# Optimization experiments

Measured on AMD Instinct MI355X. Metric: run time of the kernel, lower is better.

The kernel has to match this reference:

```python
import jax, jax.numpy as jnp
from jax import lax
import numpy as np

NUM_BLOCKS = 50
HIDDEN = 16
KERNEL = 9  # padding = 4 -> 'SAME' for stride 1
B, H, W = 16, 128, 128


def setup_inputs() -> dict:
    key = jax.random.key(0)
    k0, k1, k2, k3, k4 = jax.random.split(key, 5)
    x = jax.random.normal(k0, (B, 1, H, W), jnp.float32)
    # Stacked per-block params; block i uses w1[i, :, :1+i] (rest is padding, never read)
    w1 = jax.random.normal(k1, (NUM_BLOCKS, HIDDEN, 1 + NUM_BLOCKS, KERNEL, KERNEL), jnp.float32) * 0.05
    b1 = jax.random.normal(k2, (NUM_BLOCKS, HIDDEN), jnp.float32) * 0.05
    w2 = jax.random.normal(k3, (NUM_BLOCKS, HIDDEN), jnp.float32) * 0.05  # 1x1 conv to 1 channel
    b2 = jax.random.normal(k4, (NUM_BLOCKS,), jnp.float32) * 0.05
    return {"x": x, "w1": w1, "b1": b1, "w2": w2, "b2": b2}


def reference(x, w1, b1, w2, b2):
    # DenseNet-style growing concat: block i consumes concat of x and all previous outputs.
    feats = x  # [B, 1+i, H, W] at block i
    outs = []
    for i in range(NUM_BLOCKS):
        wi = w1[i, :, : 1 + i]  # [HIDDEN, 1+i, K, K]
        h = lax.conv_general_dilated(
            feats, wi, window_strides=(1, 1), padding="SAME",
            dimension_numbers=("NCHW", "OIHW", "NCHW"))
        h = jax.nn.relu(h + b1[i][None, :, None, None])  # [B, HIDDEN, H, W]
        # 1x1 conv to a single channel + sigmoid
        y = jax.nn.sigmoid(jnp.einsum("bchw,c->bhw", h, w2[i])[:, None] + b2[i])  # [B,1,H,W]
        outs.append(y)
        feats = jnp.concatenate([feats, y], axis=1)
    # Original returns a list of 50 [B,1,H,W] tensors; concatenate along channel dim.
    return jnp.concatenate(outs, axis=1)  # [B, NUM_BLOCKS, H, W]
```

## Files before the change

### kernel.cpp

```cpp
#include <hip/hip_runtime.h>
#include <hip/hip_bf16.h>

#define NBLK 50
#define HID  16
#define BATCH 16
#define HH 128
#define WW 128
#define PH 136
#define PW 136
#define NCH 2
#define PXS 32
#define ROWE (PW*PXS)
#define TAPE 512

typedef __attribute__((ext_vector_type(8))) short short8;
typedef __attribute__((ext_vector_type(4))) float floatx4;

static __device__ __forceinline__ unsigned short f2bf(float f) {
    unsigned int u = __float_as_uint(f);
    unsigned int r = (u + 0x7fffu + ((u >> 16) & 1u)) >> 16;
    return (unsigned short)r;
}

static __device__ __forceinline__ int uswz(int v) { return v ^ ((v >> 3) & 7); }
static __device__ __forceinline__ int swz(int px, int kg) { return uswz(px * 4 + kg); }

#define GLD16(gp, lp) __builtin_amdgcn_global_load_lds( \
    (__attribute__((address_space(1))) void*)(void*)(gp), \
    (__attribute__((address_space(3))) void*)(lp), 16, 0, 0)

static __device__ __forceinline__ void stage_row_u(
    const unsigned short* g, unsigned short* l, int tid,
    int NU, int sh, int um1) {
    #pragma unroll
    for (int t = 0; t < 3; ++t) {
        int j = t * 256 + tid;
        if (j < NU) {
            int v  = uswz(j);
            int pg = ((v >> sh) << 2) + (v & um1);
            GLD16((const char*)g + (size_t)uswz(pg) * 16,
                  (char*)l + (size_t)(t * 256 + (tid & ~63)) * 16);
        }
    }
}

__global__ void prep_w(const float* __restrict__ w1, unsigned short* __restrict__ wbuf) {
    int idx = blockIdx.x * 256 + threadIdx.x;
    const int total = NBLK * NCH * 81 * TAPE;
    if (idx >= total) return;
    int e    = idx & 7;
    int lane = (idx >> 3) & 63;
    int slot = (idx >> 9) % 81;
    int bc   = idx / (81 * TAPE);
    int ch   = bc & 1, blk = bc >> 1;
    int hc   = lane & 15, kg = lane >> 4;
    int Kc = blk + 1 - 32 * ch;
    if (Kc > 32) Kc = 32;
    float v = 0.f;
    if (Kc >= 1) {
        int kgs = (Kc + 7) >> 3;
        int sh  = (kgs >= 3) ? 2 : (kgs >> 1);
        int P   = 4 >> sh;
        int ky  = slot / 9, q = slot % 9;
        int kx  = q * P + (kg >> sh);
        int cl  = (kg & ((1 << sh) - 1)) * 8 + e;
        int c   = ch * 32 + cl;
        if (kx <= 8 && c <= blk)
            v = w1[(((size_t)blk * HID + hc) * (1 + NBLK) + c) * 81 + ky * 9 + kx];
    }
    wbuf[idx] = f2bf(v);
}

__global__ void zero_halo(unsigned short* __restrict__ feats) {
    int t = blockIdx.x * 256 + threadIdx.x;
    const int PPX = 2112;
    const int TOT = BATCH * NCH * PPX * 4;
    if (t >= TOT) return;
    int w    = t & 3;
    int rest = t >> 2;
    int p    = rest % PPX;
    int ch   = (rest / PPX) % NCH;
    int b    = rest / (PPX * NCH);
    int row, px;
    if (p < 1088) {
        int r4 = p / 136; px = p % 136;
        row = (r4 < 4) ? r4 : r4 + 128;
    } else {
        int q = p - 1088;
        row = 4 + (q >> 3);
        int c = q & 7;
        px = (c < 4) ? c : c + 128;
    }
    float4* dst = (float4*)((char*)feats +
        ((((size_t)b * PH + row) * NCH + ch) * ROWE) * 2 + (size_t)swz(px, w) * 16);
    *dst = make_float4(0.f, 0.f, 0.f, 0.f);
}

__global__ void init_x(const float* __restrict__ x, unsigned short* __restrict__ feats) {
    int idx = blockIdx.x * 256 + threadIdx.x;
    if (idx >= BATCH * HH * WW) return;
    int xw = idx & (WW - 1);
    int yy = (idx >> 7) & (HH - 1);
    int b  = idx >> 14;
    int pp = xw + 4;
    feats[((((size_t)b * PH + (yy + 4)) * NCH)) * ROWE + (size_t)swz(pp, 0) * 8]
        = f2bf(x[idx]);
}

template<int SH>
static __device__ __forceinline__ void chunk_pass(
    const unsigned short* __restrict__ base,
    const unsigned short* __restrict__ wsrc,
    unsigned short (*sB)[ROWE],
    floatx4 (&acc)[4][2],
    int tid, int n, int kg, int x0)
{
    constexpr int P   = 4 >> SH;
    constexpr int PT  = (8 + P) / P;
    constexpr int um1 = (1 << SH) - 1;
    constexpr int NU  = 136 << SH;
    const int bvx = ((x0 + n + (kg >> SH)) << SH) + (kg & um1);
    const size_t rstride = (size_t)NCH * ROWE;

    if constexpr (SH < 2) {
        if (tid < 16)
            *(short8*)(&sB[tid >> 3][(size_t)(NU + (tid & 7)) * 8]) =
                (short8){0, 0, 0, 0, 0, 0, 0, 0};
    }

    short8 Areg[4][PT];
    stage_row_u(base, &sB[0][0], tid, NU, SH, um1);
    #pragma unroll
    for (int q = 0; q < PT; ++q)
        Areg[0][q] = *(const short8*)(wsrc + (size_t)q * TAPE);
    __syncthreads();

    #pragma unroll
    for (int step = 0; step < 12; ++step) {
        if (step < 11)
            stage_row_u(base + (size_t)(step + 1) * rstride,
                        &sB[(step + 1) & 1][0], tid, NU, SH, um1);

        const unsigned short* bb = &sB[step & 1][0];
        #pragma unroll
        for (int q = 0; q < PT; ++q) {
            short8 B0 = *(const short8*)(bb + (size_t)uswz(bvx + 4 * q) * 8);
            short8 B1 = *(const short8*)(bb + (size_t)uswz(bvx + (16 << SH) + 4 * q) * 8);
            #pragma unroll
            for (int o = 0; o < 4; ++o) {
                if (o <= step && step - o <= 8) {
                    acc[o][0] = __builtin_amdgcn_mfma_f32_16x16x32_bf16(
                        Areg[(step - o) & 3][q], B0, acc[o][0], 0, 0, 0);
                    acc[o][1] = __builtin_amdgcn_mfma_f32_16x16x32_bf16(
                        Areg[(step - o) & 3][q], B1, acc[o][1], 0, 0, 0);
                }
            }
        }

        if (step < 8) {
            #pragma unroll
            for (int q = 0; q < PT; ++q)
                Areg[(step + 1) & 3][q] =
                    *(const short8*)(wsrc + (size_t)((step + 1) * 9 + q) * TAPE);
        }
        __syncthreads();
    }
}

__global__ __launch_bounds__(256, 2) void block_kern(
    unsigned short* feats, const unsigned short* __restrict__ wbuf,
    const float* __restrict__ b1, const float* __restrict__ w2,
    const float* __restrict__ b2, float* __restrict__ out,
    int blk, int nchunk)
{
    __shared__ __align__(16) unsigned short sB[2][ROWE];

    const int xcd = blockIdx.x & 7;
    const int i   = blockIdx.x >> 3;
    const int b   = 2 * xcd + (i >> 5);
    const int s   = i & 31;

    const int tid  = threadIdx.x;
    const int lane = tid & 63;
    const int wv   = tid >> 6;
    const int n    = lane & 15;
    const int kg   = lane >> 4;
    const int x0   = wv * 32;

    floatx4 acc[4][2];
    #pragma unroll
    for (int o = 0; o < 4; ++o)
        #pragma unroll
        for (int t = 0; t < 2; ++t)
            acc[o][t] = (floatx4){0.f, 0.f, 0.f, 0.f};

    const unsigned short* fb = feats + (size_t)b * PH * NCH * ROWE;

    for (int c = 0; c < nchunk; ++c) {
        const unsigned short* wsrc = wbuf + (size_t)(blk * NCH + c) * 81 * TAPE + lane * 8;
        const unsigned short* base = fb + (size_t)((4 * s) * NCH + c) * ROWE;
        int Kc = blk + 1 - 32 * c;
        if (Kc > 32) Kc = 32;
        const int kgs = (Kc + 7) >> 3;
        if (kgs >= 3)      chunk_pass<2>(base, wsrc, sB, acc, tid, n, kg, x0);
        else if (kgs == 2) chunk_pass<1>(base, wsrc, sB, acc, tid, n, kg, x0);
        else               chunk_pass<0>(base, wsrc, sB, acc, tid, n, kg, x0);
    }

    float b1v[4], w2v[4];
    #pragma unroll
    for (int r = 0; r < 4; ++r) {
        b1v[r] = b1[blk * HID + kg * 4 + r];
        w2v[r] = w2[blk * HID + kg * 4 + r];
    }
    const float bb2 = b2[blk];
    const int cw = blk + 1, cchunk = cw >> 5, cidx = cw & 31;

    #pragma unroll
    for (int o = 0; o < 4; ++o) {
        const int yrow = 4 * s + o;
        #pragma unroll
        for (int t = 0; t < 2; ++t) {
            float p = 0.f;
            #pragma unroll
            for (int r = 0; r < 4; ++r)
                p += fmaxf(acc[o][t][r] + b1v[r], 0.f) * w2v[r];
            p += __shfl_xor(p, 16, 64);
            p += __shfl_xor(p, 32, 64);
            if (kg == 0) {
                float yv = 1.f / (1.f + __expf(-(p + bb2)));
                int px = x0 + 16 * t + n;
                out[(((size_t)b * NBLK + blk) * HH + yrow) * WW + px] = yv;
                int pp = px + 4;
                feats[(((size_t)b * PH + (yrow + 4)) * NCH + cchunk) * ROWE
                      + (size_t)swz(pp, cidx >> 3) * 8 + (cidx & 7)] = f2bf(yv);
            }
        }
    }
}

extern "C" void kernel_launch(void* const* d_in, const int* in_sizes, int n_in,
                              void* d_out, int out_size, void* d_ws, size_t ws_size,
                              hipStream_t stream) {
    const float* x  = (const float*)d_in[0];
    const float* w1 = (const float*)d_in[1];
    const float* b1 = (const float*)d_in[2];
    const float* w2 = (const float*)d_in[3];
    const float* b2 = (const float*)d_in[4];
    float* out = (float*)d_out;

    unsigned short* feats = (unsigned short*)d_ws;
    size_t feats_bytes = (size_t)BATCH * PH * NCH * ROWE * sizeof(unsigned short);
    unsigned short* wbuf = (unsigned short*)((char*)d_ws + feats_bytes);

    const int htotal = BATCH * NCH * 2112 * 4;
    zero_halo<<<(htotal + 255) / 256, 256, 0, stream>>>(feats);
    init_x<<<(BATCH * HH * WW + 255) / 256, 256, 0, stream>>>(x, feats);
    const int wtotal = NBLK * NCH * 81 * TAPE;
    prep_w<<<(wtotal + 255) / 256, 256, 0, stream>>>(w1, wbuf);

    for (int blk = 0; blk < NBLK; ++blk) {
        int nchunk = (blk + 32) / 32;
        block_kern<<<BATCH * 32, 256, 0, stream>>>(feats, wbuf, b1, w2, b2, out, blk, nchunk);
    }
}
```

Before: 1.170 ms.

## Process two input rows per barrier with a four-slot LDS ring

```diff
diff --git a/kernel.cpp b/kernel.cpp
--- a/kernel.cpp
+++ b/kernel.cpp
@@ -123,48 +123,59 @@
     const size_t rstride = (size_t)NCH * ROWE;
 
     if constexpr (SH < 2) {
-        if (tid < 16)
+        if (tid < 32)
             *(short8*)(&sB[tid >> 3][(size_t)(NU + (tid & 7)) * 8]) =
                 (short8){0, 0, 0, 0, 0, 0, 0, 0};
     }
 
     short8 Areg[4][PT];
-    stage_row_u(base, &sB[0][0], tid, NU, SH, um1);
+    stage_row_u(base,           &sB[0][0], tid, NU, SH, um1);
+    stage_row_u(base + rstride, &sB[1][0], tid, NU, SH, um1);
     #pragma unroll
     for (int q = 0; q < PT; ++q)
         Areg[0][q] = *(const short8*)(wsrc + (size_t)q * TAPE);
     __syncthreads();
 
-    #pragma unroll
-    for (int step = 0; step < 12; ++step) {
-        if (step < 11)
-            stage_row_u(base + (size_t)(step + 1) * rstride,
-                        &sB[(step + 1) & 1][0], tid, NU, SH, um1);
-
-        const unsigned short* bb = &sB[step & 1][0];
-        #pragma unroll
-        for (int q = 0; q < PT; ++q) {
-            short8 B0 = *(const short8*)(bb + (size_t)uswz(bvx + 4 * q) * 8);
-            short8 B1 = *(const short8*)(bb + (size_t)uswz(bvx + (16 << SH) + 4 * q) * 8);
-            #pragma unroll
-            for (int o = 0; o < 4; ++o) {
-                if (o <= step && step - o <= 8) {
-                    acc[o][0] = __builtin_amdgcn_mfma_f32_16x16x32_bf16(
-                        Areg[(step - o) & 3][q], B0, acc[o][0], 0, 0, 0);
-                    acc[o][1] = __builtin_amdgcn_mfma_f32_16x16x32_bf16(
-                        Areg[(step - o) & 3][q], B1, acc[o][1], 0, 0, 0);
-                }
-            }
-        }
-
-        if (step < 8) {
-            #pragma unroll
-            for (int q = 0; q < PT; ++q)
-                Areg[(step + 1) & 3][q] =
-                    *(const short8*)(wsrc + (size_t)((step + 1) * 9 + q) * TAPE);
-        }
+#define SUBSTEP(T)                                                             \
+    {                                                                          \
+        const unsigned short* bb = &sB[(T) & 3][0];                            \
+        _Pragma("unroll")                                                      \
+        for (int q = 0; q < PT; ++q) {                                         \
+            short8 B0 = *(const short8*)(bb + (size_t)uswz(bvx + 4 * q) * 8);  \
+            short8 B1 = *(const short8*)(bb +                                  \
+                (size_t)uswz(bvx + (16 << SH) + 4 * q) * 8);                   \
+            _Pragma("unroll")                                                  \
+            for (int o = 0; o < 4; ++o) {                                      \
+                if (o <= (T) && (T) - o <= 8) {                                \
+                    acc[o][0] = __builtin_amdgcn_mfma_f32_16x16x32_bf16(       \
+                        Areg[((T) - o) & 3][q], B0, acc[o][0], 0, 0, 0);       \
+                    acc[o][1] = __builtin_amdgcn_mfma_f32_16x16x32_bf16(       \
+                        Areg[((T) - o) & 3][q], B1, acc[o][1], 0, 0, 0);       \
+                }                                                              \
+            }                                                                  \
+        }                                                                      \
+        if ((T) < 8) {                                                         \
+            _Pragma("unroll")                                                  \
+            for (int q = 0; q < PT; ++q)                                       \
+                Areg[((T) + 1) & 3][q] =                                       \
+                    *(const short8*)(wsrc + (size_t)(((T) + 1) * 9 + q) * TAPE); \
+        }                                                                      \
+    }
+
+    #pragma unroll
+    for (int m = 0; m < 6; ++m) {
+        if (2 * m + 2 < 12)
+            stage_row_u(base + (size_t)(2 * m + 2) * rstride,
+                        &sB[(2 * m + 2) & 3][0], tid, NU, SH, um1);
+        if (2 * m + 3 < 12)
+            stage_row_u(base + (size_t)(2 * m + 3) * rstride,
+                        &sB[(2 * m + 3) & 3][0], tid, NU, SH, um1);
+
+        SUBSTEP(2 * m);
+        SUBSTEP(2 * m + 1);
         __syncthreads();
     }
+#undef SUBSTEP
 }
 
 __global__ __launch_bounds__(256, 2) void block_kern(
@@ -173,7 +184,7 @@
     const float* __restrict__ b2, float* __restrict__ out,
     int blk, int nchunk)
 {
-    __shared__ __align__(16) unsigned short sB[2][ROWE];
+    __shared__ __align__(16) unsigned short sB[4][ROWE];
 
     const int xcd = blockIdx.x & 7;
     const int i   = blockIdx.x >> 3;
```

New measurement: 1.196 ms. 1.02x slower.
